# Kernel tuning notes

Measured on AMD Instinct MI355X. Metric: run time of the kernel, lower is better.

The kernel has to match this reference:

```python
import math
import jax, jax.numpy as jnp
import numpy as np

NUM_BUCKETS = 32
MAX_DISTANCE = 128
N_HEADS = 16
D_KV = 64


def _relative_position_bucket(rel_pos):
    # encoder (bidirectional) path of UMT5Attention._relative_position_bucket
    num_buckets = NUM_BUCKETS // 2
    rel_buckets = (rel_pos > 0).astype(jnp.int32) * num_buckets
    rel_pos = jnp.abs(rel_pos)
    max_exact = num_buckets // 2
    is_small = rel_pos < max_exact
    # clamp to 1 inside log only to avoid nan; those entries are masked by is_small
    rel_pos_large = max_exact + (
        jnp.log(jnp.maximum(rel_pos, 1).astype(jnp.float32) / max_exact)
        / math.log(MAX_DISTANCE / max_exact)
        * (num_buckets - max_exact)
    ).astype(jnp.int32)
    rel_pos_large = jnp.minimum(rel_pos_large, num_buckets - 1)
    return rel_buckets + jnp.where(is_small, rel_pos, rel_pos_large)


def compute_bias(rel_bias, q_len, k_len):
    ctx = jnp.arange(q_len, dtype=jnp.int32)[:, None]
    mem = jnp.arange(k_len, dtype=jnp.int32)[None, :]
    bkt = _relative_position_bucket(mem - ctx)          # [q, k]
    values = rel_bias[bkt]                               # [q, k, H]
    return jnp.transpose(values, (2, 0, 1))[None]        # [1, H, q, k]


def setup_inputs() -> dict:
    key = jax.random.key(0)
    ks = jax.random.split(key, 6)
    B, S, D = 2, 2048, 1024
    s = 1.0 / math.sqrt(D)
    return {
        "hidden_states": jax.random.normal(ks[0], (B, S, D), jnp.float32),
        "attention_mask": jnp.ones((B, S), jnp.int32),
        "Wq": jax.random.normal(ks[1], (D, D), jnp.float32) * s,
        "Wk": jax.random.normal(ks[2], (D, D), jnp.float32) * s,
        "Wv": jax.random.normal(ks[3], (D, D), jnp.float32) * s,
        "Wo": jax.random.normal(ks[4], (D, D), jnp.float32) * s,
        "rel_bias": jax.random.normal(ks[5], (NUM_BUCKETS, N_HEADS), jnp.float32),
    }


def reference(hidden_states, attention_mask, Wq, Wk, Wv, Wo, rel_bias):
    b, s, _ = hidden_states.shape
    n, c = N_HEADS, D_KV
    q = (hidden_states @ Wq).reshape(b, s, n, c)
    k = (hidden_states @ Wk).reshape(b, s, n, c)
    v = (hidden_states @ Wv).reshape(b, s, n, c)
    position_bias = compute_bias(rel_bias, s, s)          # [1, H, s, s]
    mask = attention_mask[:, None, None, :]               # [b, 1, 1, s]
    position_bias = jnp.where(mask == 0,
                              jnp.finfo(hidden_states.dtype).min,
                              position_bias)
    # T5-style: no 1/sqrt(d) query scaling
    attn = jnp.einsum('binc,bjnc->bnij', q, k) + position_bias
    attn = jax.nn.softmax(attn, axis=-1)
    o = jnp.einsum('bnij,bjnc->binc', attn, v).reshape(b, s, n * c)
    return o @ Wo
```

## Files before the change

### kernel.cpp

```cpp
#include <hip/hip_runtime.h>
#include <hip/hip_bf16.h>

#define NH 16
#define DC 64
#define SEQ 2048
#define BATCH 2
#define DM 1024
#define MTOT (BATCH*SEQ)

#define LOG2E 1.44269504f
#define SMAX_BOUND 48.0f

typedef unsigned short u16;
typedef unsigned int u32;
typedef __bf16 bf16x8 __attribute__((ext_vector_type(8)));
typedef float f32x4 __attribute__((ext_vector_type(4)));
typedef int i32x4 __attribute__((ext_vector_type(4)));
typedef unsigned u32x2v __attribute__((ext_vector_type(2)));

struct __attribute__((packed, aligned(4))) f4u { f32x4 v; };

__device__ __forceinline__ u16 f2bf(float f) {
    unsigned int x = __float_as_uint(f);
    unsigned int r = (x + 0x7fffu + ((x >> 16) & 1u)) >> 16;
    return (u16)r;
}
__device__ __forceinline__ u32 cvtpk(float a, float b) {
    u32 r;
    asm("v_cvt_pk_bf16_f32 %0, %1, %2" : "=v"(r) : "v"(a), "v"(b));
    return r;
}

__device__ __forceinline__ float fexp2(float x) {
#if __has_builtin(__builtin_amdgcn_exp2f)
    return __builtin_amdgcn_exp2f(x);
#else
    return exp2f(x);
#endif
}

__device__ __forceinline__ f32x4 mfma16(bf16x8 a, bf16x8 b, f32x4 c) {
    return __builtin_amdgcn_mfma_f32_16x16x32_bf16(a, b, c, 0, 0, 0);
}

__device__ __forceinline__ void glds(const u16* g, u16* l) {
    __builtin_amdgcn_global_load_lds(
        (const __attribute__((address_space(1))) void*)g,
        (__attribute__((address_space(3))) void*)l, 16, 0, 0);
}

__device__ __forceinline__ float psum32(float v) {
    u32x2v t = __builtin_amdgcn_permlane32_swap(__float_as_uint(v), __float_as_uint(v), false, false);
    return __uint_as_float(t.x) + __uint_as_float(t.y);
}
__device__ __forceinline__ float psum16(float v) {
    u32x2v t = __builtin_amdgcn_permlane16_swap(__float_as_uint(v), __float_as_uint(v), false, false);
    return __uint_as_float(t.x) + __uint_as_float(t.y);
}


__global__ __launch_bounds__(256) void prep_kernel(
    const float* __restrict__ hs,
    const float* __restrict__ Wq, const float* __restrict__ Wk,
    const float* __restrict__ Wv, const float* __restrict__ Wo,
    const float* __restrict__ rel_bias,
    u16* __restrict__ hsb, u16* __restrict__ wT, float* __restrict__ btab)
{
    int bid = blockIdx.x, tid = threadIdx.x;
    if (bid < 4096) {
        int z = bid >> 10, rem = bid & 1023;
        int by = rem >> 5, bx = rem & 31;
        const float* W = (z == 0) ? Wq : (z == 1) ? Wk : (z == 2) ? Wv : Wo;
        float sc = (z == 0) ? LOG2E : 1.0f;
        u16* WT = wT + (size_t)z * DM * DM;
        __shared__ float tile[32][33];
        int tx = tid & 31, ty = tid >> 5;
        int kbase = by * 32, nbase = bx * 32;
#pragma unroll
        for (int i = 0; i < 4; i++)
            tile[ty * 4 + i][tx] = W[(size_t)(kbase + ty * 4 + i) * DM + nbase + tx];
        __syncthreads();
#pragma unroll
        for (int i = 0; i < 4; i++)
            WT[(size_t)(nbase + ty * 4 + i) * DM + kbase + tx] = f2bf(tile[tx][ty * 4 + i] * sc);
    } else if (bid < 6144) {
        int idx = (bid - 4096) * 256 + tid;
        int stride = 2048 * 256;
        int n4 = MTOT * DM / 4;
        for (int i = idx; i < n4; i += stride) {
            float4 v = reinterpret_cast<const float4*>(hs)[i];
            uint2 o;
            o.x = (unsigned)f2bf(v.x) | ((unsigned)f2bf(v.y) << 16);
            o.y = (unsigned)f2bf(v.z) | ((unsigned)f2bf(v.w) << 16);
            reinterpret_cast<uint2*>(hsb)[i] = o;
        }
    } else {
        int idx = (bid - 6144) * 256 + tid;
        int n = idx >> 12;
        int dpos = idx & 4095;
        int delta = dpos - 2048;
        int rb = (delta > 0) ? 16 : 0;
        int a = (delta < 0) ? -delta : delta;
        int ib;
        if (a < 8) {
            ib = a;
        } else {
            ib = 8 + (int)(logf((float)a / 8.0f) / logf(16.0f) * 8.0f);
            if (ib > 15) ib = 15;
        }
        btab[idx] = (rel_bias[(rb + ib) * NH + n] - SMAX_BOUND) * LOG2E;
    }
}

__global__ __launch_bounds__(256) void vtrans(const u16* __restrict__ V, u16* __restrict__ VT) {
    int st = blockIdx.x;
    int hb = blockIdx.y;
    const u16* src = V + ((size_t)hb * SEQ + st * 64) * DC;
    u16* dst = VT + (size_t)hb * DC * SEQ + st * 64;
    __shared__ u16 t[64][65];
    int tid = threadIdx.x;
    int r = tid >> 2, c0 = (tid & 3) * 16;
    union { bf16x8 v; u16 s[8]; } a0, a1;
    a0.v = *reinterpret_cast<const bf16x8*>(src + (size_t)r * DC + c0);
    a1.v = *reinterpret_cast<const bf16x8*>(src + (size_t)r * DC + c0 + 8);
#pragma unroll
    for (int j = 0; j < 8; j++) { t[r][c0 + j] = a0.s[j]; t[r][c0 + 8 + j] = a1.s[j]; }
    __syncthreads();
    int c = tid >> 2, s0 = (tid & 3) * 16;
    union { bf16x8 v; u16 s[8]; } o0, o1;
#pragma unroll
    for (int j = 0; j < 8; j++) { o0.s[j] = t[s0 + j][c]; o1.s[j] = t[s0 + 8 + j][c]; }
    *reinterpret_cast<bf16x8*>(dst + (size_t)c * SEQ + s0)     = o0.v;
    *reinterpret_cast<bf16x8*>(dst + (size_t)c * SEQ + s0 + 8) = o1.v;
}


template<int MODE>
__global__ __launch_bounds__(256) void gemm_bt(
    const u16* __restrict__ A, const u16* __restrict__ BT,
    u16* __restrict__ qkvout, float* __restrict__ fout)
{
    const int NTILES = DM / 128;
    const int MTILES = MTOT / 128;
    __shared__ u16 As[128 * 32];
    __shared__ u16 Bs[128 * 32];

    int nb8 = gridDim.x >> 3;
    int bid = (blockIdx.x & 7) * nb8 + (blockIdx.x >> 3);

    int proj = 0, mt, nt;
    if (MODE == 0) {
        proj = bid / (MTILES * NTILES);
        int r = bid % (MTILES * NTILES);
        mt = r / NTILES; nt = r % NTILES;
    } else {
        mt = bid / NTILES; nt = bid % NTILES;
    }
    const u16* Bp = BT + (size_t)proj * DM * DM;
    int m0 = mt * 128, n0 = nt * 128;
    int tid = threadIdx.x;
    int lane = tid & 63, wid = tid >> 6;
    int wrow = (wid >> 1) * 64, wcol = (wid & 1) * 64;

    f32x4 acc[4][4] = {};

    int srow = lane >> 2;
    int skoff = (lane & 3) * 8;

    for (int k0 = 0; k0 < DM; k0 += 32) {
        __syncthreads();
#pragma unroll
        for (int t = 0; t < 2; t++) {
            int chunk = wid * 2 + t;
            int row = chunk * 16 + srow;
            glds(A + (size_t)(m0 + row) * DM + k0 + skoff, &As[chunk * 512]);
        }
#pragma unroll
        for (int t = 0; t < 2; t++) {
            int chunk = wid * 2 + t;
            int row = chunk * 16 + srow;
            glds(Bp + (size_t)(n0 + row) * DM + k0 + skoff, &Bs[chunk * 512]);
        }
        __syncthreads();

        int ko = (lane >> 4) * 8;
        bf16x8 af[4], bfr[4];
#pragma unroll
        for (int mi = 0; mi < 4; mi++)
            af[mi] = *reinterpret_cast<const bf16x8*>(&As[(wrow + mi * 16 + (lane & 15)) * 32 + ko]);
#pragma unroll
        for (int ni = 0; ni < 4; ni++)
            bfr[ni] = *reinterpret_cast<const bf16x8*>(&Bs[(wcol + ni * 16 + (lane & 15)) * 32 + ko]);
#pragma unroll
        for (int mi = 0; mi < 4; mi++)
#pragma unroll
            for (int ni = 0; ni < 4; ni++)
                acc[mi][ni] = mfma16(af[mi], bfr[ni], acc[mi][ni]);
    }

    int rbase = (lane >> 4) * 4;
    int cidx = lane & 15;
#pragma unroll
    for (int mi = 0; mi < 4; mi++) {
#pragma unroll
        for (int ni = 0; ni < 4; ni++) {
#pragma unroll
            for (int r = 0; r < 4; r++) {
                int gm = m0 + wrow + mi * 16 + rbase + r;
                int gn = n0 + wcol + ni * 16 + cidx;
                float v = acc[mi][ni][r];
                if (MODE == 0) {
                    int b = gm >> 11, s = gm & (SEQ - 1);
                    int h = gn >> 6, c = gn & 63;
                    size_t off = (((size_t)b * NH + h) * SEQ + s) * DC + c;
                    qkvout[(size_t)proj * MTOT * DM + off] = f2bf(v);
                } else {
                    fout[(size_t)gm * DM + gn] = v;
                }
            }
        }
    }
}


__global__ __launch_bounds__(512, 4) void attn_kernel(
    const u16* __restrict__ Q, const u16* __restrict__ K, const u16* __restrict__ VT,
    const int* __restrict__ mask, const float* __restrict__ btab,
    u16* __restrict__ O)
{
    __shared__ u16 smem[16384];
    __shared__ float lds_l[4][2][16];

    int wg = blockIdx.x;
    int sw = (wg & 7) * 64 + (wg >> 3);
    int qt = sw & 15;
    int bh = sw >> 4;
    int h = bh & 15, b = bh >> 4;

    int tid = threadIdx.x, lane = tid & 63, wid = tid >> 6;
    int q15 = lane & 15, hi = lane >> 4;
    int qg = wid >> 1, kh = wid & 1;

    const u16* Qp  = Q  + (((size_t)b * NH + h) * SEQ) * DC;
    const u16* Kp  = K  + (((size_t)b * NH + h) * SEQ) * DC;
    const u16* VTp = VT + ((size_t)b * NH + h) * DC * SEQ;

    int qb = qt * 128 + qg * 32;
    int iq0 = qb + q15;
    int iq1 = qb + 16 + q15;

    bf16x8 qf00 = *reinterpret_cast<const bf16x8*>(Qp + (size_t)iq0 * DC + hi * 8);
    bf16x8 qf01 = *reinterpret_cast<const bf16x8*>(Qp + (size_t)iq0 * DC + 32 + hi * 8);
    bf16x8 qf10 = *reinterpret_cast<const bf16x8*>(Qp + (size_t)iq1 * DC + hi * 8);
    bf16x8 qf11 = *reinterpret_cast<const bf16x8*>(Qp + (size_t)iq1 * DC + 32 + hi * 8);

    int c0 = wid * 2, c1 = wid * 2 + 1;
    int lr0 = (c0 & 7) * 8 + (lane >> 3);
    int lr1 = (c1 & 7) * 8 + (lane >> 3);
    int cc0 = (lane & 7) ^ (lr0 & 7);
    int cc1 = (lane & 7) ^ (lr1 & 7);
    const u16* g0 = (wid < 4) ? (Kp + (size_t)lr0 * DC + cc0 * 8)
                              : (VTp + (size_t)lr0 * SEQ + cc0 * 8);
    const u16* g1 = (wid < 4) ? (Kp + (size_t)lr1 * DC + cc1 * 8)
                              : (VTp + (size_t)lr1 * SEQ + cc1 * 8);
    int adv = (wid < 4) ? 64 * DC : 64;
    u16* ldst0 = &smem[c0 * 512];
    u16* ldst1 = &smem[c1 * 512];

    int x0 = (hi)         ^ (q15 & 7);
    int x1 = (hi + 4)     ^ (q15 & 7);
    int xv = (kh * 4 + hi) ^ (q15 & 7);

    const float* bp0 = btab + (size_t)h * 2 * SEQ + 2048 + kh * 32 + hi * 4 - iq0;
    const float* bp1 = bp0 - 16;
    const int* mkp = mask + (size_t)b * SEQ + kh * 32 + hi * 4;

    f32x4 lv0 = {}, lv1 = {};
    f32x4 oacc[4][2] = {};

    glds(g0, ldst0);
    glds(g1, ldst1);
    const u16* pg0 = g0 + adv;
    const u16* pg1 = g1 + adv;

#pragma unroll 2
    for (int t = 0; t < SEQ / 64; t++) {
        u16* KsT = smem + ((t & 1) << 13);
        u16* VsT = KsT + 4096;
        int kt = t * 64;

        f32x4 bvm0[2], bvm1[2];
#pragma unroll
        for (int kf = 0; kf < 2; kf++) {
            f32x4 bv0 = reinterpret_cast<const f4u*>(bp0 + kt + kf * 16)->v;
            f32x4 bv1 = reinterpret_cast<const f4u*>(bp1 + kt + kf * 16)->v;
            i32x4 mv4 = *reinterpret_cast<const i32x4*>(mkp + kt + kf * 16);
#pragma unroll
            for (int r = 0; r < 4; r++) {
                bool mv = (mv4[r] != 0);
                bvm0[kf][r] = mv ? bv0[r] : -1e30f;
                bvm1[kf][r] = mv ? bv1[r] : -1e30f;
            }
        }

        if (t < SEQ / 64 - 1) {
            u16* nb = smem + (((t + 1) & 1) << 13);
            glds(pg0, &nb[c0 * 512]);
            glds(pg1, &nb[c1 * 512]);
            pg0 += adv;
            pg1 += adv;
            asm volatile("s_waitcnt vmcnt(2)" ::: "memory");
        } else {
            asm volatile("s_waitcnt vmcnt(0)" ::: "memory");
        }
        asm volatile("s_barrier" ::: "memory");

        f32x4 s0[2], s1[2];
        __builtin_amdgcn_s_setprio(1);
#pragma unroll
        for (int kf = 0; kf < 2; kf++) {
            int row = ((kh * 2 + kf) * 16 + q15) * 64;
            bf16x8 ka0 = *reinterpret_cast<const bf16x8*>(&KsT[row + x0 * 8]);
            bf16x8 ka1 = *reinterpret_cast<const bf16x8*>(&KsT[row + x1 * 8]);
            f32x4 z0 = bvm0[kf];
            z0 = mfma16(ka0, qf00, z0);
            z0 = mfma16(ka1, qf01, z0);
            s0[kf] = z0;
            f32x4 z1 = bvm1[kf];
            z1 = mfma16(ka0, qf10, z1);
            z1 = mfma16(ka1, qf11, z1);
            s1[kf] = z1;
        }
        __builtin_amdgcn_s_setprio(0);

#pragma unroll
        for (int kf = 0; kf < 2; kf++) {
#pragma unroll
            for (int r = 0; r < 4; r++) {
                s0[kf][r] = fexp2(s0[kf][r]);
                s1[kf][r] = fexp2(s1[kf][r]);
            }
            lv0 += s0[kf];
            lv1 += s1[kf];
        }

        bf16x8 pa0, pa1;
        {
            u32 cA0 = cvtpk(s0[0][0], s0[0][1]);
            u32 cA1 = cvtpk(s0[0][2], s0[0][3]);
            u32 cB0 = cvtpk(s0[1][0], s0[1][1]);
            u32 cB1 = cvtpk(s0[1][2], s0[1][3]);
            u32x2v t0 = __builtin_amdgcn_permlane32_swap(cA0, cB0, false, false);
            u32x2v t1 = __builtin_amdgcn_permlane32_swap(cA1, cB1, false, false);
            u32x2v t2 = __builtin_amdgcn_permlane16_swap(t0.x, t0.y, false, false);
            u32x2v t3 = __builtin_amdgcn_permlane16_swap(t1.x, t1.y, false, false);
            union { u32 w[4]; bf16x8 v; } up;
            up.w[0] = t2.x; up.w[1] = t3.x; up.w[2] = t2.y; up.w[3] = t3.y;
            pa0 = up.v;
        }
        {
            u32 cA0 = cvtpk(s1[0][0], s1[0][1]);
            u32 cA1 = cvtpk(s1[0][2], s1[0][3]);
            u32 cB0 = cvtpk(s1[1][0], s1[1][1]);
            u32 cB1 = cvtpk(s1[1][2], s1[1][3]);
            u32x2v t0 = __builtin_amdgcn_permlane32_swap(cA0, cB0, false, false);
            u32x2v t1 = __builtin_amdgcn_permlane32_swap(cA1, cB1, false, false);
            u32x2v t2 = __builtin_amdgcn_permlane16_swap(t0.x, t0.y, false, false);
            u32x2v t3 = __builtin_amdgcn_permlane16_swap(t1.x, t1.y, false, false);
            union { u32 w[4]; bf16x8 v; } up;
            up.w[0] = t2.x; up.w[1] = t3.x; up.w[2] = t2.y; up.w[3] = t3.y;
            pa1 = up.v;
        }

        __builtin_amdgcn_s_setprio(1);
#pragma unroll
        for (int ci = 0; ci < 4; ci++) {
            bf16x8 vf = *reinterpret_cast<const bf16x8*>(&VsT[(ci * 16 + q15) * 64 + xv * 8]);
            oacc[ci][0] = mfma16(vf, pa0, oacc[ci][0]);
            oacc[ci][1] = mfma16(vf, pa1, oacc[ci][1]);
        }
        __builtin_amdgcn_s_setprio(0);

        asm volatile("s_barrier" ::: "memory");
    }

    float l0 = (lv0[0] + lv0[1]) + (lv0[2] + lv0[3]);
    float l1 = (lv1[0] + lv1[1]) + (lv1[2] + lv1[3]);
    l0 = psum16(psum32(l0));
    l1 = psum16(psum32(l1));
    __syncthreads();

    float* fs = reinterpret_cast<float*>(smem);
    if (kh == 1) {
#pragma unroll
        for (int ci = 0; ci < 4; ci++)
#pragma unroll
            for (int qs = 0; qs < 2; qs++)
                *reinterpret_cast<f32x4*>(&fs[qg * 2048 + (ci * 2 + qs) * 256 + lane * 4]) = oacc[ci][qs];
        if (hi == 0) { lds_l[qg][0][q15] = l0; lds_l[qg][1][q15] = l1; }
    }
    __syncthreads();

    float rl0 = 0.0f, rl1 = 0.0f;
    if (kh == 0) {
#pragma unroll
        for (int ci = 0; ci < 4; ci++)
#pragma unroll
            for (int qs = 0; qs < 2; qs++)
                oacc[ci][qs] += *reinterpret_cast<const f32x4*>(&fs[qg * 2048 + (ci * 2 + qs) * 256 + lane * 4]);
        rl0 = 1.0f / (l0 + lds_l[qg][0][q15]);
        rl1 = 1.0f / (l1 + lds_l[qg][1][q15]);
    }
    __syncthreads();

    u16* Ot = smem;
    if (kh == 0) {
#pragma unroll
        for (int ci = 0; ci < 4; ci++) {
            u32 w00 = cvtpk(oacc[ci][0][0] * rl0, oacc[ci][0][1] * rl0);
            u32 w01 = cvtpk(oacc[ci][0][2] * rl0, oacc[ci][0][3] * rl0);
            int base0 = (qg * 32 + q15) * 72 + ci * 16 + hi * 4;
            *reinterpret_cast<u32*>(&Ot[base0])     = w00;
            *reinterpret_cast<u32*>(&Ot[base0 + 2]) = w01;
            u32 w10 = cvtpk(oacc[ci][1][0] * rl1, oacc[ci][1][1] * rl1);
            u32 w11 = cvtpk(oacc[ci][1][2] * rl1, oacc[ci][1][3] * rl1);
            int base1 = (qg * 32 + 16 + q15) * 72 + ci * 16 + hi * 4;
            *reinterpret_cast<u32*>(&Ot[base1])     = w10;
            *reinterpret_cast<u32*>(&Ot[base1 + 2]) = w11;
        }
    }
    __syncthreads();
    int row = tid >> 2, part = tid & 3;
    bf16x8 o0 = *reinterpret_cast<const bf16x8*>(&Ot[row * 72 + part * 16]);
    bf16x8 o1 = *reinterpret_cast<const bf16x8*>(&Ot[row * 72 + part * 16 + 8]);
    size_t ob = ((size_t)b * SEQ + qt * 128 + row) * DM + h * DC + part * 16;
    *reinterpret_cast<bf16x8*>(&O[ob])     = o0;
    *reinterpret_cast<bf16x8*>(&O[ob + 8]) = o1;
}


extern "C" void kernel_launch(void* const* d_in, const int* in_sizes, int n_in,
                              void* d_out, int out_size, void* d_ws, size_t ws_size,
                              hipStream_t stream) {
    const float* hs   = (const float*)d_in[0];
    const int*   mask = (const int*)d_in[1];
    const float* Wq   = (const float*)d_in[2];
    const float* Wk   = (const float*)d_in[3];
    const float* Wv   = (const float*)d_in[4];
    const float* Wo   = (const float*)d_in[5];
    const float* rb   = (const float*)d_in[6];

    char* ws = (char*)d_ws;
    u16* hsb  = (u16*)(ws);
    u16* wT   = (u16*)(ws + 8388608);
    u16* Qb   = (u16*)(ws + 16777216);
    u16* Ob   = (u16*)(ws + 41943040);
    float* btab = (float*)(ws + 50331648);
    float* out = (float*)d_out;

    u16* VT = hsb;

    prep_kernel<<<6400, 256, 0, stream>>>(hs, Wq, Wk, Wv, Wo, rb, hsb, wT, btab);
    gemm_bt<0><<<768, 256, 0, stream>>>(hsb, wT, Qb, nullptr);
    vtrans<<<dim3(32, 32), 256, 0, stream>>>(Qb + 2 * (size_t)MTOT * DM, VT);
    attn_kernel<<<512, 512, 0, stream>>>(
        Qb, Qb + (size_t)MTOT * DM, VT, mask, btab, Ob);
    gemm_bt<1><<<256, 256, 0, stream>>>(Ob, wT + 3 * (size_t)DM * DM, nullptr, out);
}
```

Measured before the change: 130.0 us.

## Halve attention query tile to 64 rows and double workgroup count

```diff
diff --git a/kernel.cpp b/kernel.cpp
--- a/kernel.cpp
+++ b/kernel.cpp
@@ -223,18 +223,18 @@
 }
 
 
-__global__ __launch_bounds__(512, 4) void attn_kernel(
+__global__ __launch_bounds__(512, 8) void attn_kernel(
     const u16* __restrict__ Q, const u16* __restrict__ K, const u16* __restrict__ VT,
     const int* __restrict__ mask, const float* __restrict__ btab,
     u16* __restrict__ O)
 {
     __shared__ u16 smem[16384];
-    __shared__ float lds_l[4][2][16];
+    __shared__ float lds_l[4][16];
 
     int wg = blockIdx.x;
-    int sw = (wg & 7) * 64 + (wg >> 3);
-    int qt = sw & 15;
-    int bh = sw >> 4;
+    int sw = (wg & 7) * 128 + (wg >> 3);
+    int qt = sw & 31;
+    int bh = sw >> 5;
     int h = bh & 15, b = bh >> 4;
 
     int tid = threadIdx.x, lane = tid & 63, wid = tid >> 6;
@@ -245,14 +245,10 @@
     const u16* Kp  = K  + (((size_t)b * NH + h) * SEQ) * DC;
     const u16* VTp = VT + ((size_t)b * NH + h) * DC * SEQ;
 
-    int qb = qt * 128 + qg * 32;
-    int iq0 = qb + q15;
-    int iq1 = qb + 16 + q15;
+    int iq0 = qt * 64 + qg * 16 + q15;
 
     bf16x8 qf00 = *reinterpret_cast<const bf16x8*>(Qp + (size_t)iq0 * DC + hi * 8);
     bf16x8 qf01 = *reinterpret_cast<const bf16x8*>(Qp + (size_t)iq0 * DC + 32 + hi * 8);
-    bf16x8 qf10 = *reinterpret_cast<const bf16x8*>(Qp + (size_t)iq1 * DC + hi * 8);
-    bf16x8 qf11 = *reinterpret_cast<const bf16x8*>(Qp + (size_t)iq1 * DC + 32 + hi * 8);
 
     int c0 = wid * 2, c1 = wid * 2 + 1;
     int lr0 = (c0 & 7) * 8 + (lane >> 3);
@@ -272,11 +268,10 @@
     int xv = (kh * 4 + hi) ^ (q15 & 7);
 
     const float* bp0 = btab + (size_t)h * 2 * SEQ + 2048 + kh * 32 + hi * 4 - iq0;
-    const float* bp1 = bp0 - 16;
     const int* mkp = mask + (size_t)b * SEQ + kh * 32 + hi * 4;
 
-    f32x4 lv0 = {}, lv1 = {};
-    f32x4 oacc[4][2] = {};
+    f32x4 lv0 = {};
+    f32x4 oacc[4] = {};
 
     glds(g0, ldst0);
     glds(g1, ldst1);
@@ -289,18 +284,14 @@
         u16* VsT = KsT + 4096;
         int kt = t * 64;
 
-        f32x4 bvm0[2], bvm1[2];
+        f32x4 bvm0[2];
 #pragma unroll
         for (int kf = 0; kf < 2; kf++) {
             f32x4 bv0 = reinterpret_cast<const f4u*>(bp0 + kt + kf * 16)->v;
-            f32x4 bv1 = reinterpret_cast<const f4u*>(bp1 + kt + kf * 16)->v;
             i32x4 mv4 = *reinterpret_cast<const i32x4*>(mkp + kt + kf * 16);
 #pragma unroll
-            for (int r = 0; r < 4; r++) {
-                bool mv = (mv4[r] != 0);
-                bvm0[kf][r] = mv ? bv0[r] : -1e30f;
-                bvm1[kf][r] = mv ? bv1[r] : -1e30f;
-            }
+            for (int r = 0; r < 4; r++)
+                bvm0[kf][r] = (mv4[r] != 0) ? bv0[r] : -1e30f;
         }
 
         if (t < SEQ / 64 - 1) {
@@ -315,7 +306,7 @@
         }
         asm volatile("s_barrier" ::: "memory");
 
-        f32x4 s0[2], s1[2];
+        f32x4 s0[2];
         __builtin_amdgcn_s_setprio(1);
 #pragma unroll
         for (int kf = 0; kf < 2; kf++) {
@@ -326,25 +317,18 @@
             z0 = mfma16(ka0, qf00, z0);
             z0 = mfma16(ka1, qf01, z0);
             s0[kf] = z0;
-            f32x4 z1 = bvm1[kf];
-            z1 = mfma16(ka0, qf10, z1);
-            z1 = mfma16(ka1, qf11, z1);
-            s1[kf] = z1;
         }
         __builtin_amdgcn_s_setprio(0);
 
 #pragma unroll
         for (int kf = 0; kf < 2; kf++) {
 #pragma unroll
-            for (int r = 0; r < 4; r++) {
+            for (int r = 0; r < 4; r++)
                 s0[kf][r] = fexp2(s0[kf][r]);
-                s1[kf][r] = fexp2(s1[kf][r]);
-            }
             lv0 += s0[kf];
-            lv1 += s1[kf];
-        }
-
-        bf16x8 pa0, pa1;
+        }
+
+        bf16x8 pa0;
         {
             u32 cA0 = cvtpk(s0[0][0], s0[0][1]);
             u32 cA1 = cvtpk(s0[0][2], s0[0][3]);
@@ -358,26 +342,12 @@
             up.w[0] = t2.x; up.w[1] = t3.x; up.w[2] = t2.y; up.w[3] = t3.y;
             pa0 = up.v;
         }
-        {
-            u32 cA0 = cvtpk(s1[0][0], s1[0][1]);
-            u32 cA1 = cvtpk(s1[0][2], s1[0][3]);
-            u32 cB0 = cvtpk(s1[1][0], s1[1][1]);
-            u32 cB1 = cvtpk(s1[1][2], s1[1][3]);
-            u32x2v t0 = __builtin_amdgcn_permlane32_swap(cA0, cB0, false, false);
-            u32x2v t1 = __builtin_amdgcn_permlane32_swap(cA1, cB1, false, false);
-            u32x2v t2 = __builtin_amdgcn_permlane16_swap(t0.x, t0.y, false, false);
-            u32x2v t3 = __builtin_amdgcn_permlane16_swap(t1.x, t1.y, false, false);
-            union { u32 w[4]; bf16x8 v; } up;
-            up.w[0] = t2.x; up.w[1] = t3.x; up.w[2] = t2.y; up.w[3] = t3.y;
-            pa1 = up.v;
-        }
 
         __builtin_amdgcn_s_setprio(1);
 #pragma unroll
         for (int ci = 0; ci < 4; ci++) {
             bf16x8 vf = *reinterpret_cast<const bf16x8*>(&VsT[(ci * 16 + q15) * 64 + xv * 8]);
-            oacc[ci][0] = mfma16(vf, pa0, oacc[ci][0]);
-            oacc[ci][1] = mfma16(vf, pa1, oacc[ci][1]);
+            oacc[ci] = mfma16(vf, pa0, oacc[ci]);
         }
         __builtin_amdgcn_s_setprio(0);
 
@@ -385,31 +355,24 @@
     }
 
     float l0 = (lv0[0] + lv0[1]) + (lv0[2] + lv0[3]);
-    float l1 = (lv1[0] + lv1[1]) + (lv1[2] + lv1[3]);
     l0 = psum16(psum32(l0));
-    l1 = psum16(psum32(l1));
     __syncthreads();
 
     float* fs = reinterpret_cast<float*>(smem);
     if (kh == 1) {
 #pragma unroll
         for (int ci = 0; ci < 4; ci++)
-#pragma unroll
-            for (int qs = 0; qs < 2; qs++)
-                *reinterpret_cast<f32x4*>(&fs[qg * 2048 + (ci * 2 + qs) * 256 + lane * 4]) = oacc[ci][qs];
-        if (hi == 0) { lds_l[qg][0][q15] = l0; lds_l[qg][1][q15] = l1; }
+            *reinterpret_cast<f32x4*>(&fs[qg * 1024 + ci * 256 + lane * 4]) = oacc[ci];
+        if (hi == 0) lds_l[qg][q15] = l0;
     }
     __syncthreads();
 
-    float rl0 = 0.0f, rl1 = 0.0f;
+    float rl0 = 0.0f;
     if (kh == 0) {
 #pragma unroll
         for (int ci = 0; ci < 4; ci++)
-#pragma unroll
-            for (int qs = 0; qs < 2; qs++)
-                oacc[ci][qs] += *reinterpret_cast<const f32x4*>(&fs[qg * 2048 + (ci * 2 + qs) * 256 + lane * 4]);
-        rl0 = 1.0f / (l0 + lds_l[qg][0][q15]);
-        rl1 = 1.0f / (l1 + lds_l[qg][1][q15]);
+            oacc[ci] += *reinterpret_cast<const f32x4*>(&fs[qg * 1024 + ci * 256 + lane * 4]);
+        rl0 = 1.0f / (l0 + lds_l[qg][q15]);
     }
     __syncthreads();
 
@@ -417,25 +380,18 @@
     if (kh == 0) {
 #pragma unroll
         for (int ci = 0; ci < 4; ci++) {
-            u32 w00 = cvtpk(oacc[ci][0][0] * rl0, oacc[ci][0][1] * rl0);
-            u32 w01 = cvtpk(oacc[ci][0][2] * rl0, oacc[ci][0][3] * rl0);
-            int base0 = (qg * 32 + q15) * 72 + ci * 16 + hi * 4;
+            u32 w00 = cvtpk(oacc[ci][0] * rl0, oacc[ci][1] * rl0);
+            u32 w01 = cvtpk(oacc[ci][2] * rl0, oacc[ci][3] * rl0);
+            int base0 = (qg * 16 + q15) * 72 + ci * 16 + hi * 4;
             *reinterpret_cast<u32*>(&Ot[base0])     = w00;
             *reinterpret_cast<u32*>(&Ot[base0 + 2]) = w01;
-            u32 w10 = cvtpk(oacc[ci][1][0] * rl1, oacc[ci][1][1] * rl1);
-            u32 w11 = cvtpk(oacc[ci][1][2] * rl1, oacc[ci][1][3] * rl1);
-            int base1 = (qg * 32 + 16 + q15) * 72 + ci * 16 + hi * 4;
-            *reinterpret_cast<u32*>(&Ot[base1])     = w10;
-            *reinterpret_cast<u32*>(&Ot[base1 + 2]) = w11;
         }
     }
     __syncthreads();
-    int row = tid >> 2, part = tid & 3;
-    bf16x8 o0 = *reinterpret_cast<const bf16x8*>(&Ot[row * 72 + part * 16]);
-    bf16x8 o1 = *reinterpret_cast<const bf16x8*>(&Ot[row * 72 + part * 16 + 8]);
-    size_t ob = ((size_t)b * SEQ + qt * 128 + row) * DM + h * DC + part * 16;
-    *reinterpret_cast<bf16x8*>(&O[ob])     = o0;
-    *reinterpret_cast<bf16x8*>(&O[ob + 8]) = o1;
+    int row = tid >> 3, part = tid & 7;
+    bf16x8 o0 = *reinterpret_cast<const bf16x8*>(&Ot[row * 72 + part * 8]);
+    size_t ob = ((size_t)b * SEQ + qt * 64 + row) * DM + h * DC + part * 8;
+    *reinterpret_cast<bf16x8*>(&O[ob]) = o0;
 }
 
 
@@ -463,7 +419,7 @@
     prep_kernel<<<6400, 256, 0, stream>>>(hs, Wq, Wk, Wv, Wo, rb, hsb, wT, btab);
     gemm_bt<0><<<768, 256, 0, stream>>>(hsb, wT, Qb, nullptr);
     vtrans<<<dim3(32, 32), 256, 0, stream>>>(Qb + 2 * (size_t)MTOT * DM, VT);
-    attn_kernel<<<512, 512, 0, stream>>>(
+    attn_kernel<<<1024, 512, 0, stream>>>(
         Qb, Qb + (size_t)MTOT * DM, VT, mask, btab, Ob);
     gemm_bt<1><<<256, 256, 0, stream>>>(Ob, wT + 3 * (size_t)DM * DM, nullptr, out);
 }
```

New measurement: 217.8 us. +67.5%, slower.
